# Kernel optimization log

Measured on AMD Instinct MI355X. Metric: run time of the kernel, lower is better.

## Reference

```python
import jax, jax.numpy as jnp
import numpy as np

D_MODEL = 1024
NUM_HEADS = 16
HEAD_DIM = D_MODEL // NUM_HEADS
NUM_KERNELS = 21


def tisa_bias(amp, off, sharp, seq_len):
    # amp/off/sharp: (H, K). Returns (H, L, L) translation-invariant bias.
    # Evaluate on the 2L-1 distinct relative distances, then gather (Toeplitz).
    d = jnp.arange(-(seq_len - 1), seq_len, dtype=amp.dtype)  # (2L-1,)
    # (H, K, 2L-1) -> sum over kernels -> (H, 2L-1)
    scores = jnp.sum(
        amp[:, :, None]
        * jnp.exp(-jnp.abs(sharp)[:, :, None] * (d[None, None, :] - off[:, :, None]) ** 2),
        axis=1,
    )
    i = jnp.arange(seq_len)
    rel_idx = i[None, :] - i[:, None] + (seq_len - 1)  # (L, L) in [0, 2L-2]
    return scores[:, rel_idx]  # (H, L, L)


def setup_inputs() -> dict:
    key = jax.random.key(0)
    ks = jax.random.split(key, 9)
    B, L = 4, 1024
    s = 0.02
    return {
        "x_q": jax.random.normal(ks[0], (B, L, D_MODEL), dtype=jnp.float32),
        "x_kv": jax.random.normal(ks[1], (B, L, D_MODEL), dtype=jnp.float32),
        "Wq": jax.random.normal(ks[2], (D_MODEL, D_MODEL), dtype=jnp.float32) * s,
        "Wm": jax.random.normal(ks[3], (D_MODEL, 2 * D_MODEL), dtype=jnp.float32) * s,
        "Wg": jax.random.normal(ks[4], (D_MODEL, 2 * D_MODEL), dtype=jnp.float32) * s,
        "bg": jnp.zeros((2 * D_MODEL,), dtype=jnp.float32),
        "tisa_amp": jax.random.normal(ks[5], (NUM_HEADS, NUM_KERNELS), dtype=jnp.float32) * 0.1,
        "tisa_off": jax.random.uniform(ks[6], (NUM_HEADS, NUM_KERNELS), dtype=jnp.float32, minval=-512.0, maxval=512.0),
        "tisa_sharp": jax.random.uniform(ks[7], (NUM_HEADS, NUM_KERNELS), dtype=jnp.float32, minval=1e-4, maxval=0.05),
    }


def reference(x_q, x_kv, Wq, Wm, Wg, bg, tisa_amp, tisa_off, tisa_sharp):
    B, Lq, _ = x_q.shape
    Lkv = x_kv.shape[1]
    H, Dh = NUM_HEADS, HEAD_DIM

    q = (x_q @ Wq).reshape(B, Lq, H, Dh).transpose(0, 2, 1, 3)        # (B,H,Lq,Dh)
    mem = (x_kv @ Wm)                                                 # (B,Lkv,2D)
    k = mem[..., :D_MODEL].reshape(B, Lkv, H, Dh).transpose(0, 2, 1, 3)
    v = mem[..., D_MODEL:].reshape(B, Lkv, H, Dh).transpose(0, 2, 1, 3)

    scale = 1.0 / jnp.sqrt(jnp.asarray(Dh, dtype=q.dtype))
    scores = jnp.einsum("bhqd,bhkd->bhqk", q, k) * scale              # (B,H,Lq,Lkv)
    scores = scores + tisa_bias(tisa_amp, tisa_off, tisa_sharp, Lkv)[None]
    weights = jax.nn.softmax(scores, axis=-1)

    attn = jnp.einsum("bhqk,bhkd->bhqd", weights, v)                  # (B,H,Lq,Dh)
    attn = attn.transpose(0, 2, 1, 3).reshape(B, Lq, D_MODEL)

    g = attn @ Wg + bg                                                # (B,Lq,2D)
    a, b = g[..., :D_MODEL], g[..., D_MODEL:]
    return a * jax.nn.sigmoid(b)
```

## Files before the change

kernel.cpp:

```cpp
#include <hip/hip_runtime.h>
#include <cstdint>
#include <cstddef>

typedef __attribute__((ext_vector_type(8))) short bf16x8;
typedef __attribute__((ext_vector_type(4))) float f32x4;

#define LOG2E 1.44269504f

__device__ __forceinline__ unsigned short f2bf(float x) {
  unsigned int u = __float_as_uint(x);
  u += 0x7FFFu + ((u >> 16) & 1u);
  return (unsigned short)(u >> 16);
}

__device__ __forceinline__ void gload_lds16(const void* g, void* l) {
  __builtin_amdgcn_global_load_lds(
      (const __attribute__((address_space(1))) unsigned int*)g,
      (__attribute__((address_space(3))) unsigned int*)l, 16, 0, 0);
}


__global__ void cast2_f32_bf16(const float4* __restrict__ xq,
                               const float4* __restrict__ xkv,
                               ushort4* __restrict__ dq,
                               ushort4* __restrict__ dkv) {
  int i = blockIdx.x * 256 + threadIdx.x;
  const float4* s;
  ushort4* d;
  if (i < (1 << 20)) { s = xq; d = dq; }
  else { s = xkv + ((1 << 20) * -1); d = dkv - (1 << 20); }
  float4 v = s[i];
  ushort4 o;
  o.x = f2bf(v.x); o.y = f2bf(v.y); o.z = f2bf(v.z); o.w = f2bf(v.w);
  d[i] = o;
}

__global__ void transpose_cast3(const float* __restrict__ Wq,
                                const float* __restrict__ Wm,
                                const float* __restrict__ Wg,
                                unsigned short* __restrict__ dWq,
                                unsigned short* __restrict__ dWm,
                                unsigned short* __restrict__ dWg) {
  __shared__ float tile[32][33];
  int z = blockIdx.z;
  const float* src = z == 0 ? Wq : (z == 1 ? Wm : Wg);
  unsigned short* dst = z == 0 ? dWq : (z == 1 ? dWm : dWg);
  int N = z == 0 ? 1024 : 2048;
  int nb = blockIdx.x * 32, kb = blockIdx.y * 32;
  if (nb >= N) return;
  int tx = threadIdx.x & 31, ty = threadIdx.x >> 5;
#pragma unroll
  for (int r = ty; r < 32; r += 8)
    tile[r][tx] = src[(size_t)(kb + r) * N + nb + tx];
  __syncthreads();
#pragma unroll
  for (int r = ty; r < 32; r += 8)
    dst[(size_t)(nb + r) * 1024 + kb + tx] = f2bf(tile[tx][r]);
}

__global__ void bias_tab_kernel(const float* __restrict__ amp,
                                const float* __restrict__ off,
                                const float* __restrict__ sharp,
                                float* __restrict__ tab) {
  int h = blockIdx.x;
  for (int idx = threadIdx.x; idx < 2047; idx += 256) {
    float d = (float)(idx - 1023);
    float acc = 0.f;
#pragma unroll
    for (int k = 0; k < 21; ++k) {
      float dd = d - off[h * 21 + k];
      acc += amp[h * 21 + k] * __expf(-fabsf(sharp[h * 21 + k]) * dd * dd);
    }
    tab[h * 2047 + idx] = acc * LOG2E;
  }
}


__global__ __launch_bounds__(256)
void qkv_gemm(const unsigned short* __restrict__ Xq,
              const unsigned short* __restrict__ Xkv,
              const unsigned short* __restrict__ WqT,
              const unsigned short* __restrict__ WmT,
              unsigned short* __restrict__ qbuf,
              unsigned short* __restrict__ kbuf,
              unsigned short* __restrict__ vtbuf) {
  __shared__ unsigned short sA[2][128 * 32];
  __shared__ unsigned short sB[2][128 * 32];
  const int bx = blockIdx.x;
  const bool isQ = bx < 8;
  const int ntile = (isQ ? bx : bx - 8) << 7;
  const unsigned short* A = isQ ? Xq : Xkv;
  const unsigned short* B = (isQ ? WqT : WmT) + (size_t)ntile * 1024;
  const int t = threadIdx.x, lane = t & 63, w = t >> 6;
  const int wm = (w >> 1) << 6, wn = (w & 1) << 6;
  const int mtile = blockIdx.y << 7;
  const int c = lane & 15, g = lane >> 4;
  const int srow = t >> 2, scol = (t & 3) << 3;
  const unsigned short* aP = A + (size_t)(mtile + srow) * 1024 + scol;
  const unsigned short* bP = B + (size_t)srow * 1024 + scol;
  const int lo = srow * 32 + scol;

  gload_lds16(aP, &sA[0][lo]);
  gload_lds16(aP + 64 * 1024, &sA[0][lo + 64 * 32]);
  gload_lds16(bP, &sB[0][lo]);
  gload_lds16(bP + 64 * 1024, &sB[0][lo + 64 * 32]);
  __syncthreads();

  f32x4 acc[4][4] = {};
  for (int kt = 0; kt < 32; ++kt) {
    const int cur = kt & 1;
    if (kt + 1 < 32) {
      const int ko = (kt + 1) * 32;
      gload_lds16(aP + ko, &sA[1 - cur][lo]);
      gload_lds16(aP + 64 * 1024 + ko, &sA[1 - cur][lo + 64 * 32]);
      gload_lds16(bP + ko, &sB[1 - cur][lo]);
      gload_lds16(bP + 64 * 1024 + ko, &sB[1 - cur][lo + 64 * 32]);
    }
    bf16x8 af[4], bfr[4];
#pragma unroll
    for (int i = 0; i < 4; ++i) {
      af[i]  = *(const bf16x8*)&sA[cur][(wm + i * 16 + c) * 32 + g * 8];
      bfr[i] = *(const bf16x8*)&sB[cur][(wn + i * 16 + c) * 32 + g * 8];
    }
#pragma unroll
    for (int i = 0; i < 4; ++i)
#pragma unroll
      for (int j = 0; j < 4; ++j)
        acc[i][j] = __builtin_amdgcn_mfma_f32_16x16x32_bf16(af[i], bfr[j], acc[i][j], 0, 0, 0);
    __syncthreads();
  }

  const int row0 = mtile + wm + (g << 2);
  const int col0 = ntile + wn + c;
  if (isQ) {
#pragma unroll
    for (int i = 0; i < 4; ++i)
#pragma unroll
      for (int j = 0; j < 4; ++j) {
        int r = row0 + i * 16, cl = col0 + j * 16;
#pragma unroll
        for (int ri = 0; ri < 4; ++ri)
          qbuf[(size_t)(r + ri) * 1024 + cl] = f2bf(acc[i][j][ri] * (0.125f * LOG2E));
      }
  } else {
#pragma unroll
    for (int i = 0; i < 4; ++i)
#pragma unroll
      for (int j = 0; j < 4; ++j) {
        int r = row0 + i * 16, cl = col0 + j * 16;
        if (cl < 1024) {
#pragma unroll
          for (int ri = 0; ri < 4; ++ri)
            kbuf[(size_t)(r + ri) * 1024 + cl] = f2bf(acc[i][j][ri]);
        } else {
          int d = cl - 1024;
          int hh = d >> 6, dh = d & 63;
          int bb = r >> 10, ll = r & 1023;
          ushort4 pk;
          pk.x = f2bf(acc[i][j][0]);
          pk.y = f2bf(acc[i][j][1]);
          pk.z = f2bf(acc[i][j][2]);
          pk.w = f2bf(acc[i][j][3]);
          *(ushort4*)&vtbuf[((size_t)((bb * 16 + hh) * 64 + dh) << 10) + ll] = pk;
        }
      }
  }
}


__global__ __launch_bounds__(512)
void attn_kernel(const unsigned short* __restrict__ qbuf,
                 const unsigned short* __restrict__ kbuf,
                 const unsigned short* __restrict__ vtbuf,
                 const float* __restrict__ biasTab,
                 unsigned short* __restrict__ attnb) {
  const int qt = blockIdx.x, h = blockIdx.y, b = blockIdx.z;
  __shared__ unsigned short sQ[128 * 64];
  __shared__ unsigned short sK[2][64 * 64];
  __shared__ unsigned short sV[2][64 * 64];
  __shared__ unsigned short sP[8][16 * 64];
  const int t = threadIdx.x, lane = t & 63, w = t >> 6;
  const int c = lane & 15, g = lane >> 4;

  const int r = t >> 3, pc = t & 7, ch = pc ^ (r & 7);

  const unsigned short* qsrc = qbuf + (size_t)(b * 1024 + qt * 128) * 1024 + h * 64;
  const unsigned short* ksrc = kbuf + (size_t)(b * 1024) * 1024 + h * 64;
  const unsigned short* vsrc = vtbuf + (size_t)((b * 16 + h) * 64) * 1024;

  gload_lds16(qsrc + (size_t)r * 1024 + ch * 8, &sQ[t * 8]);
  gload_lds16(qsrc + (size_t)(r + 64) * 1024 + ch * 8, &sQ[4096 + t * 8]);
  gload_lds16(ksrc + (size_t)r * 1024 + ch * 8, &sK[0][t * 8]);
  gload_lds16(vsrc + (size_t)r * 1024 + ch * 8, &sV[0][t * 8]);
  __syncthreads();

  const int qrow = w * 16 + c;
  const int qx = (qrow & 7) * 8;
  bf16x8 aq0 = *(const bf16x8*)&sQ[qrow * 64 + ((g * 8) ^ qx)];
  bf16x8 aq1 = *(const bf16x8*)&sQ[qrow * 64 + (((g + 4) * 8) ^ qx)];

  f32x4 o[4] = {};
  float lsum[4] = {0.f, 0.f, 0.f, 0.f};
  const int qrow0 = qt * 128 + w * 16 + g * 4;
  const float* bbase = biasTab + h * 2047 + 1023 + c - qrow0;

  for (int kv = 0; kv < 16; ++kv) {
    const int cur = kv & 1;
    if (kv + 1 < 16) {
      gload_lds16(ksrc + (size_t)((kv + 1) * 64 + r) * 1024 + ch * 8, &sK[1 - cur][t * 8]);
      gload_lds16(vsrc + (size_t)r * 1024 + (kv + 1) * 64 + ch * 8, &sV[1 - cur][t * 8]);
    }

    f32x4 s[4];
#pragma unroll
    for (int nf = 0; nf < 4; ++nf) {
      int krow = nf * 16 + c;
      int kx = (krow & 7) * 8;
      bf16x8 b0 = *(const bf16x8*)&sK[cur][krow * 64 + ((g * 8) ^ kx)];
      bf16x8 b1 = *(const bf16x8*)&sK[cur][krow * 64 + (((g + 4) * 8) ^ kx)];
      f32x4 z = {};
      z = __builtin_amdgcn_mfma_f32_16x16x32_bf16(aq0, b0, z, 0, 0, 0);
      z = __builtin_amdgcn_mfma_f32_16x16x32_bf16(aq1, b1, z, 0, 0, 0);
      s[nf] = z;
    }

    const float* bk = bbase + kv * 64;
#pragma unroll
    for (int nf = 0; nf < 4; ++nf)
#pragma unroll
      for (int ri = 0; ri < 4; ++ri) {
        float e = exp2f(s[nf][ri] + bk[nf * 16 - ri]);
        lsum[ri] += e;
        int prow = g * 4 + ri;
        sP[w][prow * 64 + (((2 * nf + (c >> 3)) ^ (prow & 7)) * 8) + (c & 7)] = f2bf(e);
      }

    int px = (c & 7) * 8;
    bf16x8 ap0 = *(const bf16x8*)&sP[w][c * 64 + ((g * 8) ^ px)];
    bf16x8 ap1 = *(const bf16x8*)&sP[w][c * 64 + (((g + 4) * 8) ^ px)];
#pragma unroll
    for (int nf = 0; nf < 4; ++nf) {
      int vrow = nf * 16 + c;
      int vx = (vrow & 7) * 8;
      bf16x8 b0 = *(const bf16x8*)&sV[cur][vrow * 64 + ((g * 8) ^ vx)];
      bf16x8 b1 = *(const bf16x8*)&sV[cur][vrow * 64 + (((g + 4) * 8) ^ vx)];
      o[nf] = __builtin_amdgcn_mfma_f32_16x16x32_bf16(ap0, b0, o[nf], 0, 0, 0);
      o[nf] = __builtin_amdgcn_mfma_f32_16x16x32_bf16(ap1, b1, o[nf], 0, 0, 0);
    }
    __syncthreads();
  }

#pragma unroll
  for (int off = 1; off < 16; off <<= 1)
#pragma unroll
    for (int ri = 0; ri < 4; ++ri)
      lsum[ri] += __shfl_xor(lsum[ri], off, 64);
  float rinv[4];
#pragma unroll
  for (int ri = 0; ri < 4; ++ri) rinv[ri] = 1.0f / lsum[ri];

  unsigned short* obase = attnb + (size_t)(b * 1024 + qt * 128 + w * 16 + g * 4) * 1024 + h * 64;
#pragma unroll
  for (int nf = 0; nf < 4; ++nf)
#pragma unroll
    for (int ri = 0; ri < 4; ++ri)
      obase[(size_t)ri * 1024 + nf * 16 + c] = f2bf(o[nf][ri] * rinv[ri]);
}


__global__ __launch_bounds__(256)
void out_gemm(const unsigned short* __restrict__ A,
              const unsigned short* __restrict__ WgT,
              const float* __restrict__ bg,
              float* __restrict__ out) {
  __shared__ unsigned short sA[2][128 * 32];
  __shared__ unsigned short sB[2][128 * 32];
  const int nb = blockIdx.x;
  const int mtile = blockIdx.y << 7;
  const int t = threadIdx.x, lane = t & 63, w = t >> 6;
  const int c = lane & 15, g = lane >> 4;
  const int srow = t >> 2, scol = (t & 3) << 3;
  const unsigned short* aP = A + (size_t)(mtile + srow) * 1024 + scol;
  const unsigned short* bP0 = WgT + (size_t)(nb * 64 + srow) * 1024 + scol;
  const unsigned short* bP1 = WgT + (size_t)(1024 + nb * 64 + srow) * 1024 + scol;
  const int lo = srow * 32 + scol;

  gload_lds16(aP, &sA[0][lo]);
  gload_lds16(aP + 64 * 1024, &sA[0][lo + 64 * 32]);
  gload_lds16(bP0, &sB[0][lo]);
  gload_lds16(bP1, &sB[0][lo + 64 * 32]);
  __syncthreads();

  f32x4 acc[2][8] = {};
  for (int kt = 0; kt < 32; ++kt) {
    const int cur = kt & 1;
    if (kt + 1 < 32) {
      const int ko = (kt + 1) * 32;
      gload_lds16(aP + ko, &sA[1 - cur][lo]);
      gload_lds16(aP + 64 * 1024 + ko, &sA[1 - cur][lo + 64 * 32]);
      gload_lds16(bP0 + ko, &sB[1 - cur][lo]);
      gload_lds16(bP1 + ko, &sB[1 - cur][lo + 64 * 32]);
    }
    bf16x8 af[2], bfr[8];
#pragma unroll
    for (int i = 0; i < 2; ++i)
      af[i] = *(const bf16x8*)&sA[cur][(w * 32 + i * 16 + c) * 32 + g * 8];
#pragma unroll
    for (int j = 0; j < 8; ++j)
      bfr[j] = *(const bf16x8*)&sB[cur][(j * 16 + c) * 32 + g * 8];
#pragma unroll
    for (int i = 0; i < 2; ++i)
#pragma unroll
      for (int j = 0; j < 8; ++j)
        acc[i][j] = __builtin_amdgcn_mfma_f32_16x16x32_bf16(af[i], bfr[j], acc[i][j], 0, 0, 0);
    __syncthreads();
  }

#pragma unroll
  for (int i = 0; i < 2; ++i) {
    int row0 = mtile + w * 32 + i * 16 + (g << 2);
#pragma unroll
    for (int jj = 0; jj < 4; ++jj) {
      int col = nb * 64 + jj * 16 + c;
      float ba = bg[col];
      float bb = bg[1024 + col];
#pragma unroll
      for (int ri = 0; ri < 4; ++ri) {
        float av = acc[i][jj][ri] + ba;
        float bv = acc[i][jj + 4][ri] + bb;
        out[(size_t)(row0 + ri) * 1024 + col] = av / (1.f + exp2f(-LOG2E * bv));
      }
    }
  }
}


extern "C" void kernel_launch(void* const* d_in, const int* in_sizes, int n_in,
                              void* d_out, int out_size, void* d_ws, size_t ws_size,
                              hipStream_t stream) {
  const float* x_q   = (const float*)d_in[0];
  const float* x_kv  = (const float*)d_in[1];
  const float* Wq    = (const float*)d_in[2];
  const float* Wm    = (const float*)d_in[3];
  const float* Wg    = (const float*)d_in[4];
  const float* bg    = (const float*)d_in[5];
  const float* amp   = (const float*)d_in[6];
  const float* off   = (const float*)d_in[7];
  const float* sharp = (const float*)d_in[8];
  float* out = (float*)d_out;

  char* ws = (char*)d_ws;
  size_t o = 0;
  auto alloc = [&](size_t bytes) {
    char* p = ws + o;
    o += (bytes + 255) & ~(size_t)255;
    return p;
  };
  unsigned short* bXq   = (unsigned short*)alloc(4096ull * 1024 * 2);
  unsigned short* bXkv  = (unsigned short*)alloc(4096ull * 1024 * 2);
  unsigned short* bWqT  = (unsigned short*)alloc(1024ull * 1024 * 2);
  unsigned short* bWmT  = (unsigned short*)alloc(2048ull * 1024 * 2);
  unsigned short* bWgT  = (unsigned short*)alloc(2048ull * 1024 * 2);
  float*          biasT = (float*)alloc(16ull * 2047 * 4);
  unsigned short* qbuf  = (unsigned short*)alloc(4096ull * 1024 * 2);
  unsigned short* kbuf  = (unsigned short*)alloc(4096ull * 1024 * 2);
  unsigned short* vtbuf = (unsigned short*)alloc(4096ull * 1024 * 2);
  unsigned short* attnb = (unsigned short*)alloc(4096ull * 1024 * 2);
  if (ws_size < o) return;

  cast2_f32_bf16<<<8192, 256, 0, stream>>>((const float4*)x_q, (const float4*)x_kv,
                                           (ushort4*)bXq, (ushort4*)bXkv);
  transpose_cast3<<<dim3(64, 32, 3), 256, 0, stream>>>(Wq, Wm, Wg, bWqT, bWmT, bWgT);
  bias_tab_kernel<<<16, 256, 0, stream>>>(amp, off, sharp, biasT);

  qkv_gemm<<<dim3(24, 32), 256, 0, stream>>>(bXq, bXkv, bWqT, bWmT, qbuf, kbuf, vtbuf);
  attn_kernel<<<dim3(8, 16, 4), 512, 0, stream>>>(qbuf, kbuf, vtbuf, biasT, attnb);
  out_gemm<<<dim3(16, 32), 256, 0, stream>>>(attnb, bWgT, bg, out);
}
```

Measured before the change: 222.0 us.

## Fuse preprocessing kernels and retile attention into 2x2 wave grid

Merges the three preprocessing kernels (input cast, weight transpose-cast, bias table) into one launch to cut launch overhead. Reworks the attention kernel so each wave computes a 32x32 sub-tile (2 row-frags by 2 col-frags), reusing K/V fragments across two query fragments. Q and P now share one LDS buffer, bias is preloaded as the MFMA accumulator init, and P uses truncating bf16 conversion. Row sums are combined across wave columns through LDS; it adds an extra barrier per iteration and slightly less accurate P rounding.

```diff
diff --git a/kernel.cpp b/kernel.cpp
--- a/kernel.cpp
+++ b/kernel.cpp
@@ -12,6 +12,9 @@
   u += 0x7FFFu + ((u >> 16) & 1u);
   return (unsigned short)(u >> 16);
 }
+__device__ __forceinline__ unsigned short f2bf_trunc(float x) {
+  return (unsigned short)(__float_as_uint(x) >> 16);
+}
 
 __device__ __forceinline__ void gload_lds16(const void* g, void* l) {
   __builtin_amdgcn_global_load_lds(
@@ -20,58 +23,54 @@
 }
 
 
-__global__ void cast2_f32_bf16(const float4* __restrict__ xq,
-                               const float4* __restrict__ xkv,
-                               ushort4* __restrict__ dq,
-                               ushort4* __restrict__ dkv) {
-  int i = blockIdx.x * 256 + threadIdx.x;
-  const float4* s;
-  ushort4* d;
-  if (i < (1 << 20)) { s = xq; d = dq; }
-  else { s = xkv + ((1 << 20) * -1); d = dkv - (1 << 20); }
-  float4 v = s[i];
-  ushort4 o;
-  o.x = f2bf(v.x); o.y = f2bf(v.y); o.z = f2bf(v.z); o.w = f2bf(v.w);
-  d[i] = o;
-}
-
-__global__ void transpose_cast3(const float* __restrict__ Wq,
-                                const float* __restrict__ Wm,
-                                const float* __restrict__ Wg,
-                                unsigned short* __restrict__ dWq,
-                                unsigned short* __restrict__ dWm,
-                                unsigned short* __restrict__ dWg) {
+__global__ void preproc(const float* __restrict__ x_q, const float* __restrict__ x_kv,
+                        const float* __restrict__ Wq, const float* __restrict__ Wm,
+                        const float* __restrict__ Wg,
+                        const float* __restrict__ amp, const float* __restrict__ off,
+                        const float* __restrict__ sharp,
+                        ushort4* __restrict__ bXq, ushort4* __restrict__ bXkv,
+                        unsigned short* __restrict__ dWq, unsigned short* __restrict__ dWm,
+                        unsigned short* __restrict__ dWg, float* __restrict__ tab) {
   __shared__ float tile[32][33];
-  int z = blockIdx.z;
-  const float* src = z == 0 ? Wq : (z == 1 ? Wm : Wg);
-  unsigned short* dst = z == 0 ? dWq : (z == 1 ? dWm : dWg);
-  int N = z == 0 ? 1024 : 2048;
-  int nb = blockIdx.x * 32, kb = blockIdx.y * 32;
-  if (nb >= N) return;
-  int tx = threadIdx.x & 31, ty = threadIdx.x >> 5;
-#pragma unroll
-  for (int r = ty; r < 32; r += 8)
-    tile[r][tx] = src[(size_t)(kb + r) * N + nb + tx];
-  __syncthreads();
-#pragma unroll
-  for (int r = ty; r < 32; r += 8)
-    dst[(size_t)(nb + r) * 1024 + kb + tx] = f2bf(tile[tx][r]);
-}
-
-__global__ void bias_tab_kernel(const float* __restrict__ amp,
-                                const float* __restrict__ off,
-                                const float* __restrict__ sharp,
-                                float* __restrict__ tab) {
-  int h = blockIdx.x;
-  for (int idx = threadIdx.x; idx < 2047; idx += 256) {
-    float d = (float)(idx - 1023);
-    float acc = 0.f;
-#pragma unroll
-    for (int k = 0; k < 21; ++k) {
-      float dd = d - off[h * 21 + k];
-      acc += amp[h * 21 + k] * __expf(-fabsf(sharp[h * 21 + k]) * dd * dd);
-    }
-    tab[h * 2047 + idx] = acc * LOG2E;
+  const int blk = blockIdx.x;
+  if (blk < 8192) {
+    int i = blk * 256 + threadIdx.x;
+    float4 v;
+    ushort4* d;
+    if (i < (1 << 20)) { v = ((const float4*)x_q)[i]; d = bXq + i; }
+    else { int j = i - (1 << 20); v = ((const float4*)x_kv)[j]; d = bXkv + j; }
+    ushort4 o;
+    o.x = f2bf(v.x); o.y = f2bf(v.y); o.z = f2bf(v.z); o.w = f2bf(v.w);
+    *d = o;
+  } else if (blk < 14336) {
+    int idx = blk - 8192;
+    int z = idx >> 11, rem = idx & 2047;
+    int bx = rem & 63, by = rem >> 6;
+    const float* src = z == 0 ? Wq : (z == 1 ? Wm : Wg);
+    unsigned short* dst = z == 0 ? dWq : (z == 1 ? dWm : dWg);
+    int N = z == 0 ? 1024 : 2048;
+    int nb = bx * 32, kb = by * 32;
+    if (nb >= N) return;
+    int tx = threadIdx.x & 31, ty = threadIdx.x >> 5;
+#pragma unroll
+    for (int r = ty; r < 32; r += 8)
+      tile[r][tx] = src[(size_t)(kb + r) * N + nb + tx];
+    __syncthreads();
+#pragma unroll
+    for (int r = ty; r < 32; r += 8)
+      dst[(size_t)(nb + r) * 1024 + kb + tx] = f2bf(tile[tx][r]);
+  } else {
+    int h = blk - 14336;
+    for (int idx = threadIdx.x; idx < 2047; idx += 256) {
+      float d = (float)(idx - 1023);
+      float acc = 0.f;
+#pragma unroll
+      for (int k = 0; k < 21; ++k) {
+        float dd = d - off[h * 21 + k];
+        acc += amp[h * 21 + k] * __expf(-fabsf(sharp[h * 21 + k]) * dd * dd);
+      }
+      tab[h * 2047 + idx] = acc * LOG2E;
+    }
   }
 }
 
@@ -168,103 +167,141 @@
 }
 
 
-__global__ __launch_bounds__(512)
+__global__ __launch_bounds__(512, 4)
 void attn_kernel(const unsigned short* __restrict__ qbuf,
                  const unsigned short* __restrict__ kbuf,
                  const unsigned short* __restrict__ vtbuf,
                  const float* __restrict__ biasTab,
                  unsigned short* __restrict__ attnb) {
-  const int qt = blockIdx.x, h = blockIdx.y, b = blockIdx.z;
-  __shared__ unsigned short sQ[128 * 64];
+  const int h = blockIdx.x & 15, b = blockIdx.x >> 4, qt = blockIdx.y;
   __shared__ unsigned short sK[2][64 * 64];
   __shared__ unsigned short sV[2][64 * 64];
-  __shared__ unsigned short sP[8][16 * 64];
+  __shared__ unsigned short sQP[128 * 64];
+  __shared__ float sLsum[2][128];
   const int t = threadIdx.x, lane = t & 63, w = t >> 6;
   const int c = lane & 15, g = lane >> 4;
-
-  const int r = t >> 3, pc = t & 7, ch = pc ^ (r & 7);
+  const int rg = w >> 1, cg = w & 1;
+
+  const int r = t >> 3, ch = (t & 7) ^ (r & 7);
 
   const unsigned short* qsrc = qbuf + (size_t)(b * 1024 + qt * 128) * 1024 + h * 64;
   const unsigned short* ksrc = kbuf + (size_t)(b * 1024) * 1024 + h * 64;
   const unsigned short* vsrc = vtbuf + (size_t)((b * 16 + h) * 64) * 1024;
 
-  gload_lds16(qsrc + (size_t)r * 1024 + ch * 8, &sQ[t * 8]);
-  gload_lds16(qsrc + (size_t)(r + 64) * 1024 + ch * 8, &sQ[4096 + t * 8]);
+  gload_lds16(qsrc + (size_t)r * 1024 + ch * 8, &sQP[t * 8]);
+  gload_lds16(qsrc + (size_t)(r + 64) * 1024 + ch * 8, &sQP[4096 + t * 8]);
   gload_lds16(ksrc + (size_t)r * 1024 + ch * 8, &sK[0][t * 8]);
   gload_lds16(vsrc + (size_t)r * 1024 + ch * 8, &sV[0][t * 8]);
   __syncthreads();
 
-  const int qrow = w * 16 + c;
-  const int qx = (qrow & 7) * 8;
-  bf16x8 aq0 = *(const bf16x8*)&sQ[qrow * 64 + ((g * 8) ^ qx)];
-  bf16x8 aq1 = *(const bf16x8*)&sQ[qrow * 64 + (((g + 4) * 8) ^ qx)];
-
-  f32x4 o[4] = {};
-  float lsum[4] = {0.f, 0.f, 0.f, 0.f};
-  const int qrow0 = qt * 128 + w * 16 + g * 4;
-  const float* bbase = biasTab + h * 2047 + 1023 + c - qrow0;
+  bf16x8 aq[2][2];
+#pragma unroll
+  for (int rf = 0; rf < 2; ++rf) {
+    int row = rg * 32 + rf * 16 + c;
+#pragma unroll
+    for (int ks = 0; ks < 2; ++ks)
+      aq[rf][ks] = *(const bf16x8*)&sQP[row * 64 + (((ks * 4 + g) ^ (row & 7)) * 8)];
+  }
+  __syncthreads();
+
+  f32x4 o[2][2] = {};
+  float lsum[2][4] = {};
+  const float* bb = biasTab + h * 2047 + 1023 + cg * 32 + c - qt * 128 - rg * 32 - g * 4;
 
   for (int kv = 0; kv < 16; ++kv) {
     const int cur = kv & 1;
+
+    const float* bk = bb + kv * 64;
+    f32x4 s[2][2];
+#pragma unroll
+    for (int rf = 0; rf < 2; ++rf)
+#pragma unroll
+      for (int nf = 0; nf < 2; ++nf)
+#pragma unroll
+        for (int ri = 0; ri < 4; ++ri)
+          s[rf][nf][ri] = bk[(nf - rf) * 16 - ri];
+
     if (kv + 1 < 16) {
       gload_lds16(ksrc + (size_t)((kv + 1) * 64 + r) * 1024 + ch * 8, &sK[1 - cur][t * 8]);
       gload_lds16(vsrc + (size_t)r * 1024 + (kv + 1) * 64 + ch * 8, &sV[1 - cur][t * 8]);
     }
 
-    f32x4 s[4];
-#pragma unroll
-    for (int nf = 0; nf < 4; ++nf) {
-      int krow = nf * 16 + c;
-      int kx = (krow & 7) * 8;
-      bf16x8 b0 = *(const bf16x8*)&sK[cur][krow * 64 + ((g * 8) ^ kx)];
-      bf16x8 b1 = *(const bf16x8*)&sK[cur][krow * 64 + (((g + 4) * 8) ^ kx)];
-      f32x4 z = {};
-      z = __builtin_amdgcn_mfma_f32_16x16x32_bf16(aq0, b0, z, 0, 0, 0);
-      z = __builtin_amdgcn_mfma_f32_16x16x32_bf16(aq1, b1, z, 0, 0, 0);
-      s[nf] = z;
-    }
-
-    const float* bk = bbase + kv * 64;
-#pragma unroll
-    for (int nf = 0; nf < 4; ++nf)
-#pragma unroll
-      for (int ri = 0; ri < 4; ++ri) {
-        float e = exp2f(s[nf][ri] + bk[nf * 16 - ri]);
-        lsum[ri] += e;
-        int prow = g * 4 + ri;
-        sP[w][prow * 64 + (((2 * nf + (c >> 3)) ^ (prow & 7)) * 8) + (c & 7)] = f2bf(e);
-      }
-
-    int px = (c & 7) * 8;
-    bf16x8 ap0 = *(const bf16x8*)&sP[w][c * 64 + ((g * 8) ^ px)];
-    bf16x8 ap1 = *(const bf16x8*)&sP[w][c * 64 + (((g + 4) * 8) ^ px)];
-#pragma unroll
-    for (int nf = 0; nf < 4; ++nf) {
-      int vrow = nf * 16 + c;
-      int vx = (vrow & 7) * 8;
-      bf16x8 b0 = *(const bf16x8*)&sV[cur][vrow * 64 + ((g * 8) ^ vx)];
-      bf16x8 b1 = *(const bf16x8*)&sV[cur][vrow * 64 + (((g + 4) * 8) ^ vx)];
-      o[nf] = __builtin_amdgcn_mfma_f32_16x16x32_bf16(ap0, b0, o[nf], 0, 0, 0);
-      o[nf] = __builtin_amdgcn_mfma_f32_16x16x32_bf16(ap1, b1, o[nf], 0, 0, 0);
-    }
+#pragma unroll
+    for (int nf = 0; nf < 2; ++nf) {
+      int krow = cg * 32 + nf * 16 + c;
+      bf16x8 b0 = *(const bf16x8*)&sK[cur][krow * 64 + (((g) ^ (krow & 7)) * 8)];
+      bf16x8 b1 = *(const bf16x8*)&sK[cur][krow * 64 + (((4 + g) ^ (krow & 7)) * 8)];
+#pragma unroll
+      for (int rf = 0; rf < 2; ++rf) {
+        s[rf][nf] = __builtin_amdgcn_mfma_f32_16x16x32_bf16(aq[rf][0], b0, s[rf][nf], 0, 0, 0);
+        s[rf][nf] = __builtin_amdgcn_mfma_f32_16x16x32_bf16(aq[rf][1], b1, s[rf][nf], 0, 0, 0);
+      }
+    }
+
+#pragma unroll
+    for (int rf = 0; rf < 2; ++rf)
+#pragma unroll
+      for (int nf = 0; nf < 2; ++nf)
+#pragma unroll
+        for (int ri = 0; ri < 4; ++ri) {
+          float e = exp2f(s[rf][nf][ri]);
+          lsum[rf][ri] += e;
+          int prow = rg * 32 + rf * 16 + g * 4 + ri;
+          int chunk = cg * 4 + nf * 2 + (c >> 3);
+          sQP[prow * 64 + ((chunk ^ (prow & 7)) * 8) + (c & 7)] = f2bf_trunc(e);
+        }
     __syncthreads();
+
+    bf16x8 ap[2][2];
+#pragma unroll
+    for (int rf = 0; rf < 2; ++rf) {
+      int row = rg * 32 + rf * 16 + c;
+#pragma unroll
+      for (int ks = 0; ks < 2; ++ks)
+        ap[rf][ks] = *(const bf16x8*)&sQP[row * 64 + (((ks * 4 + g) ^ (row & 7)) * 8)];
+    }
+#pragma unroll
+    for (int df = 0; df < 2; ++df) {
+      int vrow = cg * 32 + df * 16 + c;
+      bf16x8 b0 = *(const bf16x8*)&sV[cur][vrow * 64 + (((g) ^ (vrow & 7)) * 8)];
+      bf16x8 b1 = *(const bf16x8*)&sV[cur][vrow * 64 + (((4 + g) ^ (vrow & 7)) * 8)];
+#pragma unroll
+      for (int rf = 0; rf < 2; ++rf) {
+        o[rf][df] = __builtin_amdgcn_mfma_f32_16x16x32_bf16(ap[rf][0], b0, o[rf][df], 0, 0, 0);
+        o[rf][df] = __builtin_amdgcn_mfma_f32_16x16x32_bf16(ap[rf][1], b1, o[rf][df], 0, 0, 0);
+      }
+    }
+    __syncthreads();
   }
 
 #pragma unroll
   for (int off = 1; off < 16; off <<= 1)
 #pragma unroll
-    for (int ri = 0; ri < 4; ++ri)
-      lsum[ri] += __shfl_xor(lsum[ri], off, 64);
-  float rinv[4];
-#pragma unroll
-  for (int ri = 0; ri < 4; ++ri) rinv[ri] = 1.0f / lsum[ri];
-
-  unsigned short* obase = attnb + (size_t)(b * 1024 + qt * 128 + w * 16 + g * 4) * 1024 + h * 64;
-#pragma unroll
-  for (int nf = 0; nf < 4; ++nf)
-#pragma unroll
-    for (int ri = 0; ri < 4; ++ri)
-      obase[(size_t)ri * 1024 + nf * 16 + c] = f2bf(o[nf][ri] * rinv[ri]);
+    for (int rf = 0; rf < 2; ++rf)
+#pragma unroll
+      for (int ri = 0; ri < 4; ++ri)
+        lsum[rf][ri] += __shfl_xor(lsum[rf][ri], off, 64);
+  if (c == 0) {
+#pragma unroll
+    for (int rf = 0; rf < 2; ++rf)
+#pragma unroll
+      for (int ri = 0; ri < 4; ++ri)
+        sLsum[cg][rg * 32 + rf * 16 + g * 4 + ri] = lsum[rf][ri];
+  }
+  __syncthreads();
+
+  unsigned short* obase = attnb +
+      (size_t)(b * 1024 + qt * 128 + rg * 32 + g * 4) * 1024 + h * 64 + cg * 32 + c;
+#pragma unroll
+  for (int rf = 0; rf < 2; ++rf)
+#pragma unroll
+    for (int ri = 0; ri < 4; ++ri) {
+      int row = rg * 32 + rf * 16 + g * 4 + ri;
+      float rinv = 1.0f / (sLsum[0][row] + sLsum[1][row]);
+#pragma unroll
+      for (int df = 0; df < 2; ++df)
+        obase[(size_t)(rf * 16 + ri) * 1024 + df * 16] = f2bf(o[rf][df][ri] * rinv);
+    }
 }
 
 
@@ -323,11 +360,11 @@
     for (int jj = 0; jj < 4; ++jj) {
       int col = nb * 64 + jj * 16 + c;
       float ba = bg[col];
-      float bb = bg[1024 + col];
+      float bbv = bg[1024 + col];
 #pragma unroll
       for (int ri = 0; ri < 4; ++ri) {
         float av = acc[i][jj][ri] + ba;
-        float bv = acc[i][jj + 4][ri] + bb;
+        float bv = acc[i][jj + 4][ri] + bbv;
         out[(size_t)(row0 + ri) * 1024 + col] = av / (1.f + exp2f(-LOG2E * bv));
       }
     }
@@ -368,12 +405,10 @@
   unsigned short* attnb = (unsigned short*)alloc(4096ull * 1024 * 2);
   if (ws_size < o) return;
 
-  cast2_f32_bf16<<<8192, 256, 0, stream>>>((const float4*)x_q, (const float4*)x_kv,
-                                           (ushort4*)bXq, (ushort4*)bXkv);
-  transpose_cast3<<<dim3(64, 32, 3), 256, 0, stream>>>(Wq, Wm, Wg, bWqT, bWmT, bWgT);
-  bias_tab_kernel<<<16, 256, 0, stream>>>(amp, off, sharp, biasT);
-
+  preproc<<<14352, 256, 0, stream>>>(x_q, x_kv, Wq, Wm, Wg, amp, off, sharp,
+                                     (ushort4*)bXq, (ushort4*)bXkv,
+                                     bWqT, bWmT, bWgT, biasT);
   qkv_gemm<<<dim3(24, 32), 256, 0, stream>>>(bXq, bXkv, bWqT, bWmT, qbuf, kbuf, vtbuf);
-  attn_kernel<<<dim3(8, 16, 4), 512, 0, stream>>>(qbuf, kbuf, vtbuf, biasT, attnb);
+  attn_kernel<<<dim3(64, 8), 512, 0, stream>>>(qbuf, kbuf, vtbuf, biasT, attnb);
   out_gemm<<<dim3(16, 32), 256, 0, stream>>>(attnb, bWgT, bg, out);
 }
```

Result: faster. 217.6 us (-2.0%).
